# Performance work log

Measured on AMD Instinct MI355X. Metric: run time of the kernel, lower is better.

The kernel has to match this reference:

```python
import jax, jax.numpy as jnp
import numpy as np

D_H, D_G, D_PROJ = 1024, 768, 256
B, L, T = 16, 2048, 512


def setup_inputs() -> dict:
    key = jax.random.key(0)
    k1, k2, k3, k4 = jax.random.split(key, 4)
    H = jax.random.normal(k1, (B, L, D_H), dtype=jnp.float32)
    G = jax.random.normal(k2, (B, T, D_G), dtype=jnp.float32)
    attn_mask = jnp.zeros((B, L), dtype=jnp.bool_)  # True = PAD/ignore
    Wk = jax.random.normal(k3, (D_PROJ, D_H), dtype=jnp.float32) * (D_H ** -0.5)
    Wq = jax.random.normal(k4, (D_PROJ, D_G), dtype=jnp.float32) * (D_G ** -0.5)
    return {"H": H, "G": G, "attn_mask": attn_mask, "Wk": Wk, "Wq": Wq}


def reference(H, G, attn_mask, Wk, Wq):
    # K = Wk(H): (B,L,P); Q = Wq(G): (B,T,P)
    K = jnp.einsum('bld,pd->blp', H, Wk)
    Q = jnp.einsum('btd,pd->btp', G, Wq)
    scale = D_PROJ ** -0.5
    logits = jnp.einsum('btp,blp->btl', Q, K) * scale  # (B,T,L)
    neg_inf = jnp.finfo(logits.dtype).min
    logits = jnp.where(attn_mask[:, None, :], neg_inf, logits)
    alpha = jax.nn.softmax(logits, axis=-1)  # stable, equals streaming softmax
    Z = jnp.einsum('btl,bld->btd', alpha, H)  # (B,T,Dh)
    return Z
```

## Files before the change

kernel.cpp:

```cpp
#include <hip/hip_runtime.h>
#include <hip/hip_bf16.h>


static constexpr int BB = 16;
static constexpr int LL = 2048;
static constexpr int TT = 512;
static constexpr int DH = 1024;
static constexpr int DG = 768;
static constexpr int PP = 256;

typedef short s16x8 __attribute__((ext_vector_type(8)));
typedef float f32x4 __attribute__((ext_vector_type(4)));

__device__ __forceinline__ unsigned short f2bf(float f) {
  __hip_bfloat16 h = __float2bfloat16(f);
  return __builtin_bit_cast(unsigned short, h);
}

__global__ __launch_bounds__(256) void k_transpose_h(
    const float* __restrict__ H, unsigned short* __restrict__ Ht) {
  __shared__ unsigned short tile[64][68];
  const int l0 = blockIdx.x * 64;
  const int d0 = blockIdx.y * 64;
  const int b = blockIdx.z;
  const int t = threadIdx.x;
#pragma unroll
  for (int i = 0; i < 4; ++i) {
    int s = i * 256 + t;
    int l = s >> 4;
    int d = (s & 15) * 4;
    const float4 v = *reinterpret_cast<const float4*>(
        &H[(size_t)(b * LL + l0 + l) * DH + d0 + d]);
    tile[d + 0][l] = f2bf(v.x);
    tile[d + 1][l] = f2bf(v.y);
    tile[d + 2][l] = f2bf(v.z);
    tile[d + 3][l] = f2bf(v.w);
  }
  __syncthreads();
#pragma unroll
  for (int i = 0; i < 4; ++i) {
    int s = i * 256 + t;
    int d = s >> 4;
    int l = (s & 15) * 4;
    ushort4 o;
    o.x = tile[d][l + 0];
    o.y = tile[d][l + 1];
    o.z = tile[d][l + 2];
    o.w = tile[d][l + 3];
    *reinterpret_cast<ushort4*>(
        &Ht[(size_t)(b * DH + d0 + d) * LL + l0 + l]) = o;
  }
}

__global__ __launch_bounds__(256) void k_proj(
    const float* __restrict__ A, const float* __restrict__ W,
    unsigned short* __restrict__ Out, int Kd) {
  __shared__ unsigned short Al[128][72];
  __shared__ unsigned short Bl[128][72];
  const int m0 = blockIdx.x * 128;
  const int n0 = blockIdx.y * 128;
  const int tid = threadIdx.x;
  const int lane = tid & 63;
  const int wave = tid >> 6;
  const int wm = (wave & 1) * 64;
  const int wn = (wave >> 1) * 64;
  const int fr = lane & 15;
  const int fg = lane >> 4;
  f32x4 acc[4][4] = {};
  for (int k0 = 0; k0 < Kd; k0 += 64) {
    __syncthreads();
#pragma unroll
    for (int i = 0; i < 8; ++i) {
      int s = i * 256 + tid;
      int r = s >> 4;
      int c = (s & 15) * 4;
      float4 va = *reinterpret_cast<const float4*>(&A[(size_t)(m0 + r) * Kd + k0 + c]);
      ushort4 ua;
      ua.x = f2bf(va.x); ua.y = f2bf(va.y); ua.z = f2bf(va.z); ua.w = f2bf(va.w);
      *reinterpret_cast<ushort4*>(&Al[r][c]) = ua;
      float4 vb = *reinterpret_cast<const float4*>(&W[(size_t)(n0 + r) * Kd + k0 + c]);
      ushort4 ub;
      ub.x = f2bf(vb.x); ub.y = f2bf(vb.y); ub.z = f2bf(vb.z); ub.w = f2bf(vb.w);
      *reinterpret_cast<ushort4*>(&Bl[r][c]) = ub;
    }
    __syncthreads();
#pragma unroll
    for (int kk = 0; kk < 64; kk += 32) {
      s16x8 af[4], bfr[4];
#pragma unroll
      for (int mi = 0; mi < 4; ++mi)
        af[mi] = *reinterpret_cast<const s16x8*>(&Al[wm + mi * 16 + fr][kk + fg * 8]);
#pragma unroll
      for (int ni = 0; ni < 4; ++ni)
        bfr[ni] = *reinterpret_cast<const s16x8*>(&Bl[wn + ni * 16 + fr][kk + fg * 8]);
#pragma unroll
      for (int mi = 0; mi < 4; ++mi)
#pragma unroll
        for (int ni = 0; ni < 4; ++ni)
          acc[mi][ni] = __builtin_amdgcn_mfma_f32_16x16x32_bf16(af[mi], bfr[ni], acc[mi][ni], 0, 0, 0);
    }
  }
#pragma unroll
  for (int mi = 0; mi < 4; ++mi)
#pragma unroll
    for (int ni = 0; ni < 4; ++ni)
#pragma unroll
      for (int r = 0; r < 4; ++r) {
        int row = m0 + wm + mi * 16 + fg * 4 + r;
        int col = n0 + wn + ni * 16 + fr;
        Out[(size_t)row * PP + col] = f2bf(acc[mi][ni][r]);
      }
}

__global__ __launch_bounds__(256) void k_attn(
    const unsigned short* __restrict__ Qb, const unsigned short* __restrict__ Kb,
    const unsigned char* __restrict__ mask,
    unsigned short* __restrict__ E, float* __restrict__ Lsum) {
  __shared__ float red[4][16];
  const int t0 = blockIdx.x * 16;
  const int b = blockIdx.y;
  const int tid = threadIdx.x;
  const int lane = tid & 63;
  const int wave = tid >> 6;
  const int fr = lane & 15;
  const int fg = lane >> 4;
  const float C = 0.09016844005556021f;
  s16x8 qf[8];
  const unsigned short* qbase = Qb + (size_t)(b * TT + t0 + fr) * PP + fg * 8;
#pragma unroll
  for (int s = 0; s < 8; ++s)
    qf[s] = *reinterpret_cast<const s16x8*>(qbase + s * 32);
  float psum[4] = {0.f, 0.f, 0.f, 0.f};
  const int lbase = wave * 512;
  for (int fc = 0; fc < 32; ++fc) {
    const int col0 = lbase + fc * 16;
    const unsigned short* kbase = Kb + (size_t)(b * LL + col0 + fr) * PP + fg * 8;
    f32x4 acc = {0.f, 0.f, 0.f, 0.f};
#pragma unroll
    for (int s = 0; s < 8; ++s) {
      s16x8 kf = *reinterpret_cast<const s16x8*>(kbase + s * 32);
      acc = __builtin_amdgcn_mfma_f32_16x16x32_bf16(qf[s], kf, acc, 0, 0, 0);
    }
    const int col = col0 + fr;
    const bool msk = mask[b * LL + col] != 0;
#pragma unroll
    for (int r = 0; r < 4; ++r) {
      float e = msk ? 0.f : exp2f(fminf(acc[r] * C, 80.f));
      psum[r] += e;
      E[(size_t)(b * TT + t0 + fg * 4 + r) * LL + col] = f2bf(e);
    }
  }
#pragma unroll
  for (int r = 0; r < 4; ++r) {
#pragma unroll
    for (int off = 1; off < 16; off <<= 1)
      psum[r] += __shfl_xor(psum[r], off, 64);
  }
  if (fr == 0) {
#pragma unroll
    for (int r = 0; r < 4; ++r) red[wave][fg * 4 + r] = psum[r];
  }
  __syncthreads();
  if (tid < 16) {
    float s = red[0][tid] + red[1][tid] + red[2][tid] + red[3][tid];
    Lsum[b * TT + t0 + tid] = fmaxf(s, 1e-30f);
  }
}

template <bool USE_HT>
__global__ __launch_bounds__(256) void k_pv(
    const unsigned short* __restrict__ E, const unsigned short* __restrict__ Ht,
    const float* __restrict__ Hf, const float* __restrict__ Lsum,
    float* __restrict__ Z) {
  __shared__ unsigned short Al[128][72];
  __shared__ unsigned short Bl[128][72];
  const int n0 = blockIdx.x * 128;
  const int m0 = blockIdx.y * 128;
  const int b = blockIdx.z;
  const int tid = threadIdx.x;
  const int lane = tid & 63;
  const int wave = tid >> 6;
  const int wm = (wave & 1) * 64;
  const int wn = (wave >> 1) * 64;
  const int fr = lane & 15;
  const int fg = lane >> 4;
  const unsigned short* Eb = E + (size_t)b * TT * LL;
  f32x4 acc[4][4] = {};
  for (int k0 = 0; k0 < LL; k0 += 64) {
    __syncthreads();
#pragma unroll
    for (int i = 0; i < 4; ++i) {
      int s = i * 256 + tid;
      int r = s >> 3;
      int c = (s & 7) * 8;
      *reinterpret_cast<s16x8*>(&Al[r][c]) =
          *reinterpret_cast<const s16x8*>(&Eb[(size_t)(m0 + r) * LL + k0 + c]);
    }
    if (USE_HT) {
      const unsigned short* Hb = Ht + (size_t)b * DH * LL;
#pragma unroll
      for (int i = 0; i < 4; ++i) {
        int s = i * 256 + tid;
        int r = s >> 3;
        int c = (s & 7) * 8;
        *reinterpret_cast<s16x8*>(&Bl[r][c]) =
            *reinterpret_cast<const s16x8*>(&Hb[(size_t)(n0 + r) * LL + k0 + c]);
      }
    } else {
#pragma unroll
      for (int i = 0; i < 8; ++i) {
        int s = i * 256 + tid;
        int l = s >> 5;
        int d = (s & 31) * 4;
        float4 v = *reinterpret_cast<const float4*>(
            &Hf[(size_t)(b * LL + k0 + l) * DH + n0 + d]);
        Bl[d + 0][l] = f2bf(v.x);
        Bl[d + 1][l] = f2bf(v.y);
        Bl[d + 2][l] = f2bf(v.z);
        Bl[d + 3][l] = f2bf(v.w);
      }
    }
    __syncthreads();
#pragma unroll
    for (int kk = 0; kk < 64; kk += 32) {
      s16x8 af[4], bfr[4];
#pragma unroll
      for (int mi = 0; mi < 4; ++mi)
        af[mi] = *reinterpret_cast<const s16x8*>(&Al[wm + mi * 16 + fr][kk + fg * 8]);
#pragma unroll
      for (int ni = 0; ni < 4; ++ni)
        bfr[ni] = *reinterpret_cast<const s16x8*>(&Bl[wn + ni * 16 + fr][kk + fg * 8]);
#pragma unroll
      for (int mi = 0; mi < 4; ++mi)
#pragma unroll
        for (int ni = 0; ni < 4; ++ni)
          acc[mi][ni] = __builtin_amdgcn_mfma_f32_16x16x32_bf16(af[mi], bfr[ni], acc[mi][ni], 0, 0, 0);
    }
  }
#pragma unroll
  for (int mi = 0; mi < 4; ++mi)
#pragma unroll
    for (int r = 0; r < 4; ++r) {
      int row = m0 + wm + mi * 16 + fg * 4 + r;
      float inv = 1.0f / Lsum[b * TT + row];
#pragma unroll
      for (int ni = 0; ni < 4; ++ni) {
        int col = n0 + wn + ni * 16 + fr;
        Z[(size_t)(b * TT + row) * DH + col] = acc[mi][ni][r] * inv;
      }
    }
}

extern "C" void kernel_launch(void* const* d_in, const int* in_sizes, int n_in,
                              void* d_out, int out_size, void* d_ws, size_t ws_size,
                              hipStream_t stream) {
  const float* H = (const float*)d_in[0];
  const float* G = (const float*)d_in[1];
  const unsigned char* mask = (const unsigned char*)d_in[2];
  const float* Wk = (const float*)d_in[3];
  const float* Wq = (const float*)d_in[4];
  float* Z = (float*)d_out;
  char* ws = (char*)d_ws;

  const size_t OFF_KB = 0;
  const size_t OFF_QB = OFF_KB + (size_t)BB * LL * PP * 2;
  const size_t OFF_E  = OFF_QB + (size_t)BB * TT * PP * 2;
  const size_t OFF_LS = OFF_E + (size_t)BB * TT * LL * 2;
  const size_t OFF_HT = OFF_LS + (size_t)BB * TT * 4;
  const size_t WS_FULL = OFF_HT + (size_t)BB * DH * LL * 2;

  unsigned short* Kb = (unsigned short*)(ws + OFF_KB);
  unsigned short* Qb = (unsigned short*)(ws + OFF_QB);
  unsigned short* E = (unsigned short*)(ws + OFF_E);
  float* Lsum = (float*)(ws + OFF_LS);
  unsigned short* Ht = (unsigned short*)(ws + OFF_HT);

  const bool useHt = ws_size >= WS_FULL;

  if (useHt)
    k_transpose_h<<<dim3(LL / 64, DH / 64, BB), 256, 0, stream>>>(H, Ht);
  k_proj<<<dim3(BB * LL / 128, 2), 256, 0, stream>>>(H, Wk, Kb, DH);
  k_proj<<<dim3(BB * TT / 128, 2), 256, 0, stream>>>(G, Wq, Qb, DG);
  k_attn<<<dim3(TT / 16, BB), 256, 0, stream>>>(Qb, Kb, mask, E, Lsum);
  if (useHt)
    k_pv<true><<<dim3(DH / 128, TT / 128, BB), 256, 0, stream>>>(E, Ht, H, Lsum, Z);
  else
    k_pv<false><<<dim3(DH / 128, TT / 128, BB), 256, 0, stream>>>(E, Ht, H, Lsum, Z);
}
```

Baseline: 418.7 us.

## Load PV tiles via global_load_lds with pre-swizzled E and Ht layouts

The producers of E (attention) and Ht (transpose) now write with an XOR column swizzle inside each 64-element chunk. The PV kernel then streams tiles straight into LDS with global_load_lds in 16-byte pieces, skipping the register round trip, and reads MFMA fragments with matching swizzled offsets to avoid bank conflicts. The fp32-H fallback path and the workspace-size check are removed, so the code now assumes the workspace is always large enough for Ht.

```diff
diff --git a/kernel.cpp b/kernel.cpp
--- a/kernel.cpp
+++ b/kernel.cpp
@@ -15,6 +15,16 @@
 __device__ __forceinline__ unsigned short f2bf(float f) {
   __hip_bfloat16 h = __float2bfloat16(f);
   return __builtin_bit_cast(unsigned short, h);
+}
+
+__device__ __forceinline__ void gload16(const void* g, void* l) {
+  __builtin_amdgcn_global_load_lds(
+      (const __attribute__((address_space(1))) void*)g,
+      (__attribute__((address_space(3))) void*)l, 16, 0, 0);
+}
+
+__device__ __forceinline__ int swz_col(int col, int row) {
+  return (col & ~63) | ((((col >> 3) ^ row) & 7) << 3) | (col & 7);
 }
 
 __global__ __launch_bounds__(256) void k_transpose_h(
@@ -47,8 +57,10 @@
     o.y = tile[d][l + 1];
     o.z = tile[d][l + 2];
     o.w = tile[d][l + 3];
+    const int dd = d0 + d;
+    const int lp = l0 + (swz_col(l, dd & 7));
     *reinterpret_cast<ushort4*>(
-        &Ht[(size_t)(b * DH + d0 + d) * LL + l0 + l]) = o;
+        &Ht[(size_t)(b * DH + dd) * LL + lp]) = o;
   }
 }
 
@@ -147,7 +159,9 @@
     for (int r = 0; r < 4; ++r) {
       float e = msk ? 0.f : exp2f(fminf(acc[r] * C, 80.f));
       psum[r] += e;
-      E[(size_t)(b * TT + t0 + fg * 4 + r) * LL + col] = f2bf(e);
+      const int t = t0 + fg * 4 + r;
+      const int colp = swz_col(col, t & 7);
+      E[(size_t)(b * TT + t) * LL + colp] = f2bf(e);
     }
   }
 #pragma unroll
@@ -167,13 +181,11 @@
   }
 }
 
-template <bool USE_HT>
 __global__ __launch_bounds__(256) void k_pv(
     const unsigned short* __restrict__ E, const unsigned short* __restrict__ Ht,
-    const float* __restrict__ Hf, const float* __restrict__ Lsum,
-    float* __restrict__ Z) {
-  __shared__ unsigned short Al[128][72];
-  __shared__ unsigned short Bl[128][72];
+    const float* __restrict__ Lsum, float* __restrict__ Z) {
+  __shared__ __align__(16) unsigned short Al[128 * 64];
+  __shared__ __align__(16) unsigned short Bl[128 * 64];
   const int n0 = blockIdx.x * 128;
   const int m0 = blockIdx.y * 128;
   const int b = blockIdx.z;
@@ -184,52 +196,39 @@
   const int wn = (wave >> 1) * 64;
   const int fr = lane & 15;
   const int fg = lane >> 4;
+  const int fr7 = fr & 7;
   const unsigned short* Eb = E + (size_t)b * TT * LL;
+  const unsigned short* Hb = Ht + (size_t)b * DH * LL;
   f32x4 acc[4][4] = {};
   for (int k0 = 0; k0 < LL; k0 += 64) {
     __syncthreads();
 #pragma unroll
     for (int i = 0; i < 4; ++i) {
-      int s = i * 256 + tid;
-      int r = s >> 3;
-      int c = (s & 7) * 8;
-      *reinterpret_cast<s16x8*>(&Al[r][c]) =
-          *reinterpret_cast<const s16x8*>(&Eb[(size_t)(m0 + r) * LL + k0 + c]);
-    }
-    if (USE_HT) {
-      const unsigned short* Hb = Ht + (size_t)b * DH * LL;
-#pragma unroll
-      for (int i = 0; i < 4; ++i) {
-        int s = i * 256 + tid;
-        int r = s >> 3;
-        int c = (s & 7) * 8;
-        *reinterpret_cast<s16x8*>(&Bl[r][c]) =
-            *reinterpret_cast<const s16x8*>(&Hb[(size_t)(n0 + r) * LL + k0 + c]);
-      }
-    } else {
-#pragma unroll
-      for (int i = 0; i < 8; ++i) {
-        int s = i * 256 + tid;
-        int l = s >> 5;
-        int d = (s & 31) * 4;
-        float4 v = *reinterpret_cast<const float4*>(
-            &Hf[(size_t)(b * LL + k0 + l) * DH + n0 + d]);
-        Bl[d + 0][l] = f2bf(v.x);
-        Bl[d + 1][l] = f2bf(v.y);
-        Bl[d + 2][l] = f2bf(v.z);
-        Bl[d + 3][l] = f2bf(v.w);
-      }
+      const int j = i * 256 + tid;
+      const int r = j >> 3;
+      const int c8 = (j & 7) * 8;
+      char* ldsA = (char*)Al + i * 4096 + wave * 1024;
+      char* ldsB = (char*)Bl + i * 4096 + wave * 1024;
+      gload16(&Eb[(size_t)(m0 + r) * LL + k0 + c8], ldsA);
+      gload16(&Hb[(size_t)(n0 + r) * LL + k0 + c8], ldsB);
     }
     __syncthreads();
 #pragma unroll
     for (int kk = 0; kk < 64; kk += 32) {
+      const int kkd = kk >> 3;
       s16x8 af[4], bfr[4];
 #pragma unroll
-      for (int mi = 0; mi < 4; ++mi)
-        af[mi] = *reinterpret_cast<const s16x8*>(&Al[wm + mi * 16 + fr][kk + fg * 8]);
-#pragma unroll
-      for (int ni = 0; ni < 4; ++ni)
-        bfr[ni] = *reinterpret_cast<const s16x8*>(&Bl[wn + ni * 16 + fr][kk + fg * 8]);
+      for (int mi = 0; mi < 4; ++mi) {
+        const int row = wm + mi * 16 + fr;
+        const int q = ((kkd + fg) ^ fr7) << 3;
+        af[mi] = *reinterpret_cast<const s16x8*>(&Al[row * 64 + q]);
+      }
+#pragma unroll
+      for (int ni = 0; ni < 4; ++ni) {
+        const int row = wn + ni * 16 + fr;
+        const int q = ((kkd + fg) ^ fr7) << 3;
+        bfr[ni] = *reinterpret_cast<const s16x8*>(&Bl[row * 64 + q]);
+      }
 #pragma unroll
       for (int mi = 0; mi < 4; ++mi)
 #pragma unroll
@@ -267,7 +266,6 @@
   const size_t OFF_E  = OFF_QB + (size_t)BB * TT * PP * 2;
   const size_t OFF_LS = OFF_E + (size_t)BB * TT * LL * 2;
   const size_t OFF_HT = OFF_LS + (size_t)BB * TT * 4;
-  const size_t WS_FULL = OFF_HT + (size_t)BB * DH * LL * 2;
 
   unsigned short* Kb = (unsigned short*)(ws + OFF_KB);
   unsigned short* Qb = (unsigned short*)(ws + OFF_QB);
@@ -275,15 +273,9 @@
   float* Lsum = (float*)(ws + OFF_LS);
   unsigned short* Ht = (unsigned short*)(ws + OFF_HT);
 
-  const bool useHt = ws_size >= WS_FULL;
-
-  if (useHt)
-    k_transpose_h<<<dim3(LL / 64, DH / 64, BB), 256, 0, stream>>>(H, Ht);
+  k_transpose_h<<<dim3(LL / 64, DH / 64, BB), 256, 0, stream>>>(H, Ht);
   k_proj<<<dim3(BB * LL / 128, 2), 256, 0, stream>>>(H, Wk, Kb, DH);
   k_proj<<<dim3(BB * TT / 128, 2), 256, 0, stream>>>(G, Wq, Qb, DG);
   k_attn<<<dim3(TT / 16, BB), 256, 0, stream>>>(Qb, Kb, mask, E, Lsum);
-  if (useHt)
-    k_pv<true><<<dim3(DH / 128, TT / 128, BB), 256, 0, stream>>>(E, Ht, H, Lsum, Z);
-  else
-    k_pv<false><<<dim3(DH / 128, TT / 128, BB), 256, 0, stream>>>(E, Ht, H, Lsum, Z);
-}
+  k_pv<<<dim3(DH / 128, TT / 128, BB), 256, 0, stream>>>(E, Ht, Lsum, Z);
+}
```

New measurement: 428.3 us. 2.3% more time.
